# Kernel tuning notes

Measured on AMD Instinct MI355X. Metric: run time of the kernel, lower is better.

## Reference

```python
import jax, jax.numpy as jnp
import numpy as np

B, HW, E = 64, 14, 512   # batch, feature-map side, encoder_dim
A = D = M = 512          # attention_dim, decoder_dim, embed_dim
V = 1000                 # vocab_size
L = 257                  # max caption length -> T = 256 decode steps


def setup_inputs() -> dict:
    key = jax.random.key(0)
    ks = jax.random.split(key, 16)
    def w(k, shape, s=0.05):
        return jax.random.normal(k, shape, dtype=jnp.float32) * s
    encoder_out = jax.random.normal(ks[0], (B, HW, HW, E), dtype=jnp.float32)
    encoded_captions = jax.random.randint(ks[1], (B, L), 0, V)
    caption_lengths = jax.random.randint(ks[2], (B, 1), 2, L + 1)
    caption_lengths = caption_lengths.at[0, 0].set(L)  # ensure max(decode_lengths) == L-1
    return dict(
        encoder_out=encoder_out,
        encoded_captions=encoded_captions,
        caption_lengths=caption_lengths,
        emb=w(ks[3], (V, M), 0.1),
        enc_att_w=w(ks[4], (A, E)), enc_att_b=jnp.zeros((A,), jnp.float32),
        dec_att_w=w(ks[5], (A, D)), dec_att_b=jnp.zeros((A,), jnp.float32),
        full_att_w=w(ks[6], (1, A)), full_att_b=jnp.zeros((1,), jnp.float32),
        W_ih=w(ks[7], (4 * D, M + E)), b_ih=jnp.zeros((4 * D,), jnp.float32),
        W_hh=w(ks[8], (4 * D, D)), b_hh=jnp.zeros((4 * D,), jnp.float32),
        init_h_w=w(ks[9], (D, E)), init_h_b=jnp.zeros((D,), jnp.float32),
        init_c_w=w(ks[10], (D, E)), init_c_b=jnp.zeros((D,), jnp.float32),
        f_beta_w=w(ks[11], (E, D)), f_beta_b=jnp.zeros((E,), jnp.float32),
        fc_w=w(ks[12], (V, D), 0.1), fc_b=jnp.zeros((V,), jnp.float32),
    )


def _forward(encoder_out, emb, enc_att_w, enc_att_b, dec_att_w, dec_att_b,
             full_att_w, full_att_b, W_ih, b_ih, W_hh, b_hh,
             init_h_w, init_h_b, init_c_w, init_c_b,
             f_beta_w, f_beta_b, fc_w, fc_b,
             encoded_captions, caption_lengths):
    Bn = encoder_out.shape[0]
    En = encoder_out.shape[-1]
    enc = encoder_out.reshape(Bn, -1, En)            # [B, P, E]
    lens = caption_lengths[:, 0]
    sort_ind = jnp.argsort(-lens)                    # descending caption length
    lens = lens[sort_ind]
    enc = enc[sort_ind]
    caps = encoded_captions[sort_ind]
    embs = emb[caps]                                 # [B, L, M]
    mean_enc = enc.mean(axis=1)
    h0 = mean_enc @ init_h_w.T + init_h_b            # [B, D]
    c0 = mean_enc @ init_c_w.T + init_c_b
    att1 = enc @ enc_att_w.T + enc_att_b             # [B, P, A] (loop-invariant)
    dec_len = lens - 1
    T = caps.shape[1] - 1
    embs_seq = jnp.transpose(embs[:, :T, :], (1, 0, 2))  # [T, B, M]

    def step(carry, xs):
        h, c = carry
        t, emb_t = xs
        # soft attention (full batch; torch slices to active rows, masked below)
        att2 = h @ dec_att_w.T + dec_att_b                                   # [B, A]
        e = jnp.einsum('bpa,a->bp', jax.nn.relu(att1 + att2[:, None, :]),
                       full_att_w[0]) + full_att_b[0]                        # [B, P]
        alpha = jax.nn.softmax(e, axis=1)
        awe = jnp.einsum('bpe,bp->be', enc, alpha)                           # [B, E]
        gate = jax.nn.sigmoid(h @ f_beta_w.T + f_beta_b)
        x = jnp.concatenate([emb_t, gate * awe], axis=1)                     # [B, M+E]
        # LSTMCell
        gates = x @ W_ih.T + b_ih + h @ W_hh.T + b_hh
        i, f, g, o = jnp.split(gates, 4, axis=1)
        c_new = jax.nn.sigmoid(f) * c + jax.nn.sigmoid(i) * jnp.tanh(g)
        h_new = jax.nn.sigmoid(o) * jnp.tanh(c_new)
        m = (t < dec_len).astype(h.dtype)[:, None]                           # active mask
        h2 = m * h_new + (1 - m) * h
        c2 = m * c_new + (1 - m) * c
        preds = (h_new @ fc_w.T + fc_b) * m   # dropout is identity in eval
        return (h2, c2), (preds, alpha * m)

    (_, _), (preds, alphas) = jax.lax.scan(step, (h0, c0), (jnp.arange(T), embs_seq))
    predictions = jnp.transpose(preds, (1, 0, 2))   # [B, T, V]
    alphas = jnp.transpose(alphas, (1, 0, 2))       # [B, T, P]
    return predictions, caps, alphas, sort_ind


def reference(encoder_out, encoded_captions, caption_lengths, emb,
              enc_att_w, enc_att_b, dec_att_w, dec_att_b, full_att_w, full_att_b,
              W_ih, b_ih, W_hh, b_hh, init_h_w, init_h_b, init_c_w, init_c_b,
              f_beta_w, f_beta_b, fc_w, fc_b):
    return _forward(encoder_out, emb, enc_att_w, enc_att_b, dec_att_w, dec_att_b,
                    full_att_w, full_att_b, W_ih, b_ih, W_hh, b_hh,
                    init_h_w, init_h_b, init_c_w, init_c_b,
                    f_beta_w, f_beta_b, fc_w, fc_b,
                    encoded_captions, caption_lengths)
```

## Files before the change

### kernel.cpp

```cpp
#include <hip/hip_runtime.h>
#include <cstdint>
#include <cstddef>

#define NBLK 256
#define NTHR 512
#define B_ 64
#define P_ 196
#define E_ 512
#define A_ 512
#define D_ 512
#define M_ 512
#define V_ 1000
#define L_ 257
#define T_ 256

#define OUT_PRED  0
#define OUT_CAPS  (B_*T_*V_)
#define OUT_ALPHA (OUT_CAPS + B_*L_)
#define OUT_SORT  (OUT_ALPHA + B_*T_*P_)

typedef _Float16 h2 __attribute__((ext_vector_type(2)));
typedef _Float16 f16x8 __attribute__((ext_vector_type(8)));
typedef float f32x4 __attribute__((ext_vector_type(4)));

struct KP {
  const float* enc; const int* caps; const int* clen;
  const float* emb;
  const float* eaw; const float* eab;
  const float* daw; const float* dab;
  const float* faw; const float* fab;
  const float* wih; const float* bih;
  const float* whh; const float* bhh;
  const float* ihw; const float* ihb;
  const float* icw; const float* icb;
  const float* fbw; const float* fbb;
  const float* fcw; const float* fcb;
  float* out;
  int* bar; int* flb; int* gf;
  int* sort_ind; int* dec_len;
  float* mnT; float* hA; float* hB; float* hnG;
  float* a2G; float* gateG; float* aweQ; float* eG; float* att1;
};

__device__ __forceinline__ float sigf(float x){ return 1.f/(1.f+__expf(-x)); }
__device__ __forceinline__ float tanhf_(float x){
  float ax = fabsf(x);
  float e = __expf(-2.f*ax);
  float r = (1.f-e)/(1.f+e);
  return x < 0.f ? -r : r;
}
__device__ __forceinline__ unsigned short f2bf(float x){
  unsigned u = __float_as_uint(x);
  unsigned r = (u + 0x7fffu + ((u >> 16) & 1u)) >> 16;
  return (unsigned short)r;
}
__device__ __forceinline__ float fdot2f(h2 a, h2 b, float c){
#if __has_builtin(__builtin_amdgcn_fdot2)
  return __builtin_amdgcn_fdot2(a, b, c, false);
#else
  return c + (float)a.x*(float)b.x + (float)a.y*(float)b.y;
#endif
}
__device__ __forceinline__ unsigned packh2(float a, float b){
  h2 v; v.x = (_Float16)a; v.y = (_Float16)b;
  return __builtin_bit_cast(unsigned, v);
}
__device__ __forceinline__ h2 ash2(unsigned u){ return __builtin_bit_cast(h2, u); }
__device__ __forceinline__ f16x8 asf8(uint4 u){ return __builtin_bit_cast(f16x8, u); }

#define LD_A(p)     __hip_atomic_load((p), __ATOMIC_RELAXED, __HIP_MEMORY_SCOPE_AGENT)
#define ST_A(p,v)   __hip_atomic_store((p),(v), __ATOMIC_RELAXED, __HIP_MEMORY_SCOPE_AGENT)
#define ST_REL(p,v) __hip_atomic_store((p),(v), __ATOMIC_RELEASE, __HIP_MEMORY_SCOPE_AGENT)
#define FAA(p)      __hip_atomic_fetch_add((p),1, __ATOMIC_RELAXED, __HIP_MEMORY_SCOPE_AGENT)
__device__ __forceinline__ float ldg_c(const float* p){
  return __hip_atomic_load(p, __ATOMIC_RELAXED, __HIP_MEMORY_SCOPE_AGENT);
}
__device__ __forceinline__ float2 ldg2_c(const float* p){
  unsigned long long u = __hip_atomic_load((const unsigned long long*)p,
                       __ATOMIC_RELAXED, __HIP_MEMORY_SCOPE_AGENT);
  return __builtin_bit_cast(float2, u);
}
__device__ __forceinline__ void stg_c(float* p, float v){
  __hip_atomic_store(p, v, __ATOMIC_RELAXED, __HIP_MEMORY_SCOPE_AGENT);
}

__device__ __forceinline__ void gridbar(int* bar, int blk){
  __syncthreads();
  if (threadIdx.x == 0){
    __builtin_amdgcn_fence(__ATOMIC_RELEASE, "agent");
    int s = LD_A(&bar[144]);
    int* leaf = &bar[(blk & 7)*16];
    if (FAA(leaf) == 31){
      ST_A(leaf, 0);
      if (FAA(&bar[128]) == 7){
        ST_A(&bar[128], 0);
        ST_REL(&bar[144], s+1);
      }
    }
    while (LD_A(&bar[144]) == s) __builtin_amdgcn_s_sleep(2);
    __builtin_amdgcn_fence(__ATOMIC_ACQUIRE, "agent");
  }
  __syncthreads();
}

__device__ __forceinline__ void octbar(int* fl, int O, int r, int ep){
  __syncthreads();
  if (threadIdx.x == 0) ST_A(&fl[O*64 + r], ep);
  if (threadIdx.x < 32){
    while (LD_A(&fl[O*64 + (int)threadIdx.x]) < ep) __builtin_amdgcn_s_sleep(2);
  }
  asm volatile("" ::: "memory");
  __syncthreads();
}

template<int KSW>
__device__ __forceinline__ void gemv_regs(const uint4 (&wfr)[4][KSW],
                                          const uint4* __restrict__ x4,
                                          float* redW, int lane, int wave){
  f32x4 d0 = {0.f,0.f,0.f,0.f}, d1 = d0, d2 = d0, d3 = d0;
  const int rowc = lane & 7;
  const int lg = lane >> 4;
  #pragma unroll
  for (int ks = 0; ks < KSW; ks++){
    const int ksg = wave*KSW + ks;
    f16x8 bf = asf8(x4[(ksg*4 + lg)*8 + rowc]);
    d0 = __builtin_amdgcn_mfma_f32_16x16x32_f16(asf8(wfr[0][ks]), bf, d0, 0, 0, 0);
    d1 = __builtin_amdgcn_mfma_f32_16x16x32_f16(asf8(wfr[1][ks]), bf, d1, 0, 0, 0);
    d2 = __builtin_amdgcn_mfma_f32_16x16x32_f16(asf8(wfr[2][ks]), bf, d2, 0, 0, 0);
    d3 = __builtin_amdgcn_mfma_f32_16x16x32_f16(asf8(wfr[3][ks]), bf, d3, 0, 0, 0);
  }
  const int j = lane & 15;
  if (j < 8){
    const int ib = (lane >> 4) * 4;
    #pragma unroll
    for (int r = 0; r < 4; r++){
      redW[wave*512 + (( 0 + ib + r)*8) + j] = d0[r];
      redW[wave*512 + ((16 + ib + r)*8) + j] = d1[r];
      redW[wave*512 + ((32 + ib + r)*8) + j] = d2[r];
      redW[wave*512 + ((48 + ib + r)*8) + j] = d3[r];
    }
  }
}

__global__ __launch_bounds__(NTHR, 2) void dec_kernel(KP p){
  __shared__ __align__(16) char smem_raw[151104];
  unsigned short* att1L = (unsigned short*)smem_raw;
  unsigned* encT2  = (unsigned*)(smem_raw + 50176);
  float* fwL       = (float*)(smem_raw + 105472);
  float* cL        = (float*)(smem_raw + 107520);
  int*   sbL       = (int*)(smem_raw + 108032);
  char* SCR        = smem_raw + 108096;
  uint4* xH8_4     = (uint4*)SCR;
  float* redW      = (float*)(SCR + 24576);
  float* gLs       = (float*)(SCR + 40960);
  float* a2L       = (float*)SCR;
  float* gateL     = (float*)(SCR + 2048);
  float* eL        = (float*)(SCR + 4096);
  float* alphaL    = (float*)(SCR + 5120);
  unsigned* alpha2L= (unsigned*)(SCR + 6144);

  const int blk  = blockIdx.x;
  const int tid  = threadIdx.x;
  const int lane = tid & 63;
  const int wave = tid >> 6;
  const int b    = blk >> 2;
  const int q    = blk & 3;
  const int ct   = blk & 31;
  const int bt   = blk >> 5;

  if (blk == 0){
    if (tid < B_){
      int lb = p.clen[tid];
      int rank = 0;
      for (int j = 0; j < B_; j++){
        int lj = p.clen[j];
        rank += (lj > lb) || (lj == lb && j < tid);
      }
      p.sort_ind[rank] = tid;
      p.dec_len[rank]  = lb - 1;
      p.out[OUT_SORT + rank] = (float)tid;
    }
    __syncthreads();
    for (int idx = tid; idx < B_*L_; idx += NTHR){
      int bb = idx / L_;
      int l = idx - bb*L_;
      int sbv = p.sort_ind[bb];
      p.out[OUT_CAPS + idx] = (float)p.caps[sbv*L_ + l];
    }
  }
  gridbar(p.bar, blk);

  const int sb  = p.sort_ind[b];
  const int dlb = p.dec_len[b];

  for (int task = blk; task < 260; task += NBLK){
    if (task < 196){
      const int r0 = task*64;
      float* wL = (float*)smem_raw;
      float* eLt = (float*)smem_raw + 512*33;
      const int tx = tid & 31, ty = tid >> 5;
      float acc[4][16];
      #pragma unroll
      for (int i=0;i<4;i++)
        #pragma unroll
        for (int j=0;j<16;j++) acc[i][j] = 0.f;
      for (int k0 = 0; k0 < 512; k0 += 32){
        __syncthreads();
        for (int i = tid; i < 512*32; i += NTHR){
          int a = i >> 5, kk = i & 31;
          wL[a*33 + kk] = p.eaw[a*512 + k0 + kk];
        }
        for (int i = tid; i < 64*32; i += NTHR){
          int rl = i >> 5, kk = i & 31;
          int r = r0 + rl;
          int bb = r / 196;
          int pp = r - bb*196;
          int sbv = p.sort_ind[bb];
          eLt[rl*33 + kk] = p.enc[((size_t)sbv*196 + pp)*512 + k0 + kk];
        }
        __syncthreads();
        for (int kk = 0; kk < 32; kk++){
          float ev[4];
          #pragma unroll
          for (int ii=0;ii<4;ii++) ev[ii] = eLt[(ty*4+ii)*33 + kk];
          #pragma unroll
          for (int jj=0;jj<16;jj++){
            float wv = wL[(tx + 32*jj)*33 + kk];
            #pragma unroll
            for (int ii=0;ii<4;ii++) acc[ii][jj] = fmaf(ev[ii], wv, acc[ii][jj]);
          }
        }
      }
      #pragma unroll
      for (int jj=0;jj<16;jj++){
        int a = tx + 32*jj;
        float bbv = p.eab[a];
        #pragma unroll
        for (int ii=0;ii<4;ii++){
          int r = r0 + ty*4 + ii;
          p.att1[(size_t)r*512 + a] = acc[ii][jj] + bbv;
        }
      }
      __syncthreads();
    } else {
      int bb = task - 196;
      int sbv = p.sort_ind[bb];
      const float* eb = p.enc + (size_t)sbv*P_*E_;
      for (int e = tid; e < E_; e += NTHR){
        float s = 0.f;
        for (int pp = 0; pp < P_; pp++) s += eb[pp*E_ + e];
        p.mnT[bb*512 + e] = s * (1.f/196.f);
      }
    }
  }
  gridbar(p.bar, blk);

  for (int idx = tid; idx < 49*512; idx += NTHR){
    int pp = idx >> 9, a = idx & 511;
    att1L[idx] = f2bf(p.att1[((size_t)(b*196 + q*49 + pp))*512 + a]);
  }
  for (int i = tid; i < 512*25; i += NTHR){
    int p2 = i >> 9, e = i & 511;
    int pr0 = q*49 + 2*p2;
    float e0 = p.enc[((size_t)sb*196 + pr0)*512 + e];
    float e1 = (2*p2+1 < 49) ? p.enc[((size_t)sb*196 + pr0 + 1)*512 + e] : 0.f;
    encT2[e*27 + p2] = packh2(e0, e1);
  }
  fwL[tid] = p.faw[tid];
  if (tid < 8)       sbL[tid]     = p.sort_ind[bt*8 + tid];
  else if (tid < 16) sbL[tid]     = p.dec_len[bt*8 + (tid-8)];
  uint4 wa[4][2];
  uint4 wg[4][6];
  {
    const int cgb = ct*64 + (lane & 15);
    const int kof = (lane >> 4) << 3;
    #pragma unroll
    for (int mt = 0; mt < 4; mt++){
      int cg = cgb + mt*16;
      #pragma unroll
      for (int ks = 0; ks < 2; ks++){
        int k = (wave*2 + ks)*32 + kof;
        uint4 o = {0u,0u,0u,0u};
        const float* src = nullptr;
        if (cg < 512)        src = p.daw + (size_t)cg*512 + k;
        else if (cg < 1024)  src = p.fbw + (size_t)(cg-512)*512 + k;
        else if (cg < 2024)  src = p.fcw + (size_t)(cg-1024)*512 + k;
        if (src){
          const float4* s4 = (const float4*)src;
          float4 f0 = s4[0], f1 = s4[1];
          o.x = packh2(f0.x,f0.y); o.y = packh2(f0.z,f0.w);
          o.z = packh2(f1.x,f1.y); o.w = packh2(f1.z,f1.w);
        }
        wa[mt][ks] = o;
      }
      int jj = cg >> 2, g = cg & 3;
      #pragma unroll
      for (int ks = 0; ks < 6; ks++){
        int k = (wave*6 + ks)*32 + kof;
        const float* src = (k < 1024) ? p.wih + (size_t)(g*512+jj)*1024 + k
                                      : p.whh + (size_t)(g*512+jj)*512 + (k-1024);
        const float4* s4 = (const float4*)src;
        float4 f0 = s4[0], f1 = s4[1];
        uint4 o;
        o.x = packh2(f0.x,f0.y); o.y = packh2(f0.z,f0.w);
        o.z = packh2(f1.x,f1.y); o.w = packh2(f1.z,f1.w);
        wg[mt][ks] = o;
      }
    }
  }
  if (tid < 128){
    int jj = tid >> 3, bb2 = tid & 7;
    int b8 = bt*8 + bb2, jg = ct*16 + jj;
    const float* mrow = p.mnT + b8*512;
    const float* hw = p.ihw + (size_t)jg*512;
    const float* cw = p.icw + (size_t)jg*512;
    float ah = 0.f, ac = 0.f;
    for (int k = 0; k < 512; k++){ ah = fmaf(hw[k], mrow[k], ah); ac = fmaf(cw[k], mrow[k], ac); }
    stg_c(&p.hA[b8*512 + jg], ah + p.ihb[jg]);
    cL[jj*8 + bb2] = ac + p.icb[jg];
  }
  gridbar(p.bar, blk);

  const float fab0 = p.fab[0];
  int ep = 0;

  for (int t = 0; t < T_; t++){
    const float* hR = (t & 1) ? p.hB : p.hA;
    float*       hW = (t & 1) ? p.hA : p.hB;

    if (ct < 16 || t > 0){
      {
        const float* xsrc = (ct < 16) ? hR : p.hnG;
        int cc = tid >> 3, r = tid & 7;
        const float* src = xsrc + (size_t)(bt*8 + r)*512 + cc*8;
        float2 v0 = ldg2_c(src), v1 = ldg2_c(src+2), v2 = ldg2_c(src+4), v3 = ldg2_c(src+6);
        uint4 o;
        o.x = packh2(v0.x,v0.y); o.y = packh2(v1.x,v1.y);
        o.z = packh2(v2.x,v2.y); o.w = packh2(v3.x,v3.y);
        xH8_4[tid] = o;
      }
      __syncthreads();
      gemv_regs<2>(wa, xH8_4, redW, lane, wave);
      __syncthreads();
      {
        float s = 0.f;
        #pragma unroll
        for (int w8 = 0; w8 < 8; w8++) s += redW[w8*512 + tid];
        int c_local = tid >> 3, j = tid & 7, b8 = bt*8 + j;
        if (ct < 16){
          int vcl = ct*64 + c_local;
          if (vcl < 512) stg_c(&p.a2G[b8*512 + vcl], s + p.dab[vcl]);
          else           stg_c(&p.gateG[b8*512 + (vcl-512)], sigf(s + p.fbb[vcl-512]));
        } else {
          int v2i = (ct-16)*64 + c_local;
          if (v2i < 1000){
            bool mm = (t-1) < sbL[8 + j];
            p.out[OUT_PRED + ((size_t)b8*T_ + (t-1))*V_ + v2i] = mm ? (s + p.fcb[v2i]) : 0.f;
          }
        }
      }
    }
    octbar(p.flb, bt, ct, ++ep);

    {
      a2L[tid]   = ldg_c(&p.a2G[b*512 + tid]);
      gateL[tid] = ldg_c(&p.gateG[b*512 + tid]);
      __syncthreads();
      {
        float4 aA = ((float4*)a2L)[lane*2], aB = ((float4*)a2L)[lane*2+1];
        float4 fA = ((float4*)fwL)[lane*2], fB = ((float4*)fwL)[lane*2+1];
        for (int pp = wave; pp < 49; pp += 8){
          uint4 raw = ((const uint4*)att1L)[pp*64 + lane];
          float s =
            fmaxf(__uint_as_float(raw.x << 16)        + aA.x, 0.f)*fA.x +
            fmaxf(__uint_as_float(raw.x & 0xffff0000u)+ aA.y, 0.f)*fA.y +
            fmaxf(__uint_as_float(raw.y << 16)        + aA.z, 0.f)*fA.z +
            fmaxf(__uint_as_float(raw.y & 0xffff0000u)+ aA.w, 0.f)*fA.w +
            fmaxf(__uint_as_float(raw.z << 16)        + aB.x, 0.f)*fB.x +
            fmaxf(__uint_as_float(raw.z & 0xffff0000u)+ aB.y, 0.f)*fB.y +
            fmaxf(__uint_as_float(raw.w << 16)        + aB.z, 0.f)*fB.z +
            fmaxf(__uint_as_float(raw.w & 0xffff0000u)+ aB.w, 0.f)*fB.w;
          #pragma unroll
          for (int o = 32; o > 0; o >>= 1) s += __shfl_down(s, o);
          if (lane == 0) stg_c(&p.eG[b*256 + q*49 + pp], s + fab0);
        }
      }
      __syncthreads();
      if (tid == 0) ST_A(&p.gf[b*16 + q], t+1);
      if (tid < 4){
        while (LD_A(&p.gf[b*16 + tid]) < t+1) __builtin_amdgcn_s_sleep(1);
      }
      asm volatile("" ::: "memory");
      __syncthreads();
      if (tid < 196) eL[tid] = ldg_c(&p.eG[b*256 + tid]);
      __syncthreads();
      if (wave == 0){
        float mx = -1e30f;
        for (int i = lane; i < P_; i += 64) mx = fmaxf(mx, eL[i]);
        #pragma unroll
        for (int o = 32; o > 0; o >>= 1) mx = fmaxf(mx, __shfl_xor(mx, o));
        float sum = 0.f;
        for (int i = lane; i < P_; i += 64){
          float ex = __expf(eL[i] - mx);
          alphaL[i] = ex;
          sum += ex;
        }
        #pragma unroll
        for (int o = 32; o > 0; o >>= 1) sum += __shfl_xor(sum, o);
        float inv = 1.f / sum;
        for (int i = lane; i < P_; i += 64) alphaL[i] *= inv;
      }
      __syncthreads();
      {
        bool mb = t < dlb;
        if (tid < 49)
          p.out[OUT_ALPHA + ((size_t)b*T_ + t)*P_ + q*49 + tid] = mb ? alphaL[q*49 + tid] : 0.f;
        if (tid < 25){
          float a0 = alphaL[q*49 + 2*tid];
          float a1 = (2*tid+1 < 49) ? alphaL[q*49 + 2*tid + 1] : 0.f;
          alpha2L[tid] = packh2(a0, a1);
        }
      }
      __syncthreads();
      {
        const unsigned* ec = encT2 + tid*27;
        float s = 0.f;
        #pragma unroll 5
        for (int p2 = 0; p2 < 25; p2++)
          s = fdot2f(ash2(ec[p2]), ash2(alpha2L[p2]), s);
        stg_c(&p.aweQ[((size_t)b*4 + q)*512 + tid], gateL[tid]*s);
      }
    }
    octbar(p.flb, bt, ct, ++ep);

    {
      {
        int cc = tid >> 3, r = tid & 7;
        int b8 = bt*8 + r;
        {
          int cap = p.caps[sbL[r]*L_ + t];
          const float4* er = (const float4*)(p.emb + (size_t)cap*M_ + cc*8);
          float4 f0 = er[0], f1 = er[1];
          uint4 o;
          o.x = packh2(f0.x,f0.y); o.y = packh2(f0.z,f0.w);
          o.z = packh2(f1.x,f1.y); o.w = packh2(f1.z,f1.w);
          xH8_4[tid] = o;
        }
        {
          const float* aw = p.aweQ + (size_t)b8*4*512 + cc*8;
          float a8[8];
          #pragma unroll
          for (int e = 0; e < 8; e += 2){
            float2 q0 = ldg2_c(aw + 0*512 + e);
            float2 q1 = ldg2_c(aw + 1*512 + e);
            float2 q2 = ldg2_c(aw + 2*512 + e);
            float2 q3 = ldg2_c(aw + 3*512 + e);
            a8[e]   = (q0.x + q1.x) + (q2.x + q3.x);
            a8[e+1] = (q0.y + q1.y) + (q2.y + q3.y);
          }
          uint4 o;
          o.x = packh2(a8[0],a8[1]); o.y = packh2(a8[2],a8[3]);
          o.z = packh2(a8[4],a8[5]); o.w = packh2(a8[6],a8[7]);
          xH8_4[512 + tid] = o;
        }
        {
          const float* hs = hR + (size_t)b8*512 + cc*8;
          float2 v0 = ldg2_c(hs), v1 = ldg2_c(hs+2), v2 = ldg2_c(hs+4), v3 = ldg2_c(hs+6);
          uint4 o;
          o.x = packh2(v0.x,v0.y); o.y = packh2(v1.x,v1.y);
          o.z = packh2(v2.x,v2.y); o.w = packh2(v3.x,v3.y);
          xH8_4[1024 + tid] = o;
        }
      }
      __syncthreads();
      gemv_regs<6>(wg, xH8_4, redW, lane, wave);
      __syncthreads();
      {
        float s = 0.f;
        #pragma unroll
        for (int w8 = 0; w8 < 8; w8++) s += redW[w8*512 + tid];
        gLs[(tid & 7)*64 + (tid >> 3)] = s;
      }
      __syncthreads();
      if (tid < 128){
        int jj = tid >> 3, bb2 = tid & 7;
        int b8 = bt*8 + bb2, jg = ct*16 + jj;
        float g0 = gLs[bb2*64 + jj*4+0] + p.bih[jg]        + p.bhh[jg];
        float g1 = gLs[bb2*64 + jj*4+1] + p.bih[512 + jg]  + p.bhh[512 + jg];
        float g2 = gLs[bb2*64 + jj*4+2] + p.bih[1024 + jg] + p.bhh[1024 + jg];
        float g3 = gLs[bb2*64 + jj*4+3] + p.bih[1536 + jg] + p.bhh[1536 + jg];
        float i_s = sigf(g0), f_s = sigf(g1), g_t = tanhf_(g2), o_s = sigf(g3);
        float c_old = cL[jj*8 + bb2];
        float c_new = f_s*c_old + i_s*g_t;
        float h_new = o_s*tanhf_(c_new);
        bool m = t < sbL[8 + bb2];
        float h_old = ldg_c(&hR[b8*512 + jg]);
        cL[jj*8 + bb2] = m ? c_new : c_old;
        stg_c(&p.hnG[b8*512 + jg], h_new);
        stg_c(&hW[b8*512 + jg], m ? h_new : h_old);
      }
    }
    octbar(p.flb, bt, ct, ++ep);
  }

  if (ct >= 16){
    {
      int cc = tid >> 3, r = tid & 7;
      const float* src = p.hnG + (size_t)(bt*8 + r)*512 + cc*8;
      float2 v0 = ldg2_c(src), v1 = ldg2_c(src+2), v2 = ldg2_c(src+4), v3 = ldg2_c(src+6);
      uint4 o;
      o.x = packh2(v0.x,v0.y); o.y = packh2(v1.x,v1.y);
      o.z = packh2(v2.x,v2.y); o.w = packh2(v3.x,v3.y);
      xH8_4[tid] = o;
    }
    __syncthreads();
    gemv_regs<2>(wa, xH8_4, redW, lane, wave);
    __syncthreads();
    {
      float s = 0.f;
      #pragma unroll
      for (int w8 = 0; w8 < 8; w8++) s += redW[w8*512 + tid];
      int c_local = tid >> 3, j = tid & 7, b8 = bt*8 + j;
      int v2i = (ct-16)*64 + c_local;
      if (v2i < 1000){
        bool mm = (T_-1) < sbL[8 + j];
        p.out[OUT_PRED + ((size_t)b8*T_ + (T_-1))*V_ + v2i] = mm ? (s + p.fcb[v2i]) : 0.f;
      }
    }
  }
}

extern "C" void kernel_launch(void* const* d_in, const int* in_sizes, int n_in,
                              void* d_out, int out_size, void* d_ws, size_t ws_size,
                              hipStream_t stream){
  (void)in_sizes; (void)n_in; (void)out_size; (void)ws_size;
  KP p;
  p.enc  = (const float*)d_in[0];
  p.caps = (const int*)  d_in[1];
  p.clen = (const int*)  d_in[2];
  p.emb  = (const float*)d_in[3];
  p.eaw  = (const float*)d_in[4];  p.eab = (const float*)d_in[5];
  p.daw  = (const float*)d_in[6];  p.dab = (const float*)d_in[7];
  p.faw  = (const float*)d_in[8];  p.fab = (const float*)d_in[9];
  p.wih  = (const float*)d_in[10]; p.bih = (const float*)d_in[11];
  p.whh  = (const float*)d_in[12]; p.bhh = (const float*)d_in[13];
  p.ihw  = (const float*)d_in[14]; p.ihb = (const float*)d_in[15];
  p.icw  = (const float*)d_in[16]; p.icb = (const float*)d_in[17];
  p.fbw  = (const float*)d_in[18]; p.fbb = (const float*)d_in[19];
  p.fcw  = (const float*)d_in[20]; p.fcb = (const float*)d_in[21];
  p.out  = (float*)d_out;

  char* ws = (char*)d_ws;
  size_t off = 0;
  p.bar = (int*)(ws + off); off += 1024;
  p.flb = (int*)(ws + off); off += 8*64*4;
  p.gf  = (int*)(ws + off); off += 64*16*4;
  size_t zero_bytes = off;
  p.sort_ind = (int*)(ws + off); off += 64*4;
  p.dec_len  = (int*)(ws + off); off += 64*4;
  off = (off + 255) & ~(size_t)255;
  p.mnT   = (float*)(ws + off); off += (size_t)B_*512*4;
  p.hA    = (float*)(ws + off); off += (size_t)B_*512*4;
  p.hB    = (float*)(ws + off); off += (size_t)B_*512*4;
  p.hnG   = (float*)(ws + off); off += (size_t)B_*512*4;
  p.a2G   = (float*)(ws + off); off += (size_t)B_*512*4;
  p.gateG = (float*)(ws + off); off += (size_t)B_*512*4;
  p.aweQ  = (float*)(ws + off); off += (size_t)B_*4*512*4;
  p.eG    = (float*)(ws + off); off += (size_t)B_*256*4;
  p.att1  = (float*)(ws + off); off += (size_t)B_*P_*A_*4;

  hipMemsetAsync(ws, 0, zero_bytes, stream);

  void* args[] = { (void*)&p };
  hipLaunchCooperativeKernel((const void*)dec_kernel,
                             dim3(NBLK), dim3(NTHR), args, 0, stream);
}
```

Baseline: 5.617 ms.

## Split-softmax attention to drop per-step quarter barrier; store hidden state as fp16

```diff
diff --git a/kernel.cpp b/kernel.cpp
--- a/kernel.cpp
+++ b/kernel.cpp
@@ -36,10 +36,11 @@
   const float* fbw; const float* fbb;
   const float* fcw; const float* fcb;
   float* out;
-  int* bar; int* flb; int* gf;
+  int* bar; int* flb;
   int* sort_ind; int* dec_len;
-  float* mnT; float* hA; float* hB; float* hnG;
-  float* a2G; float* gateG; float* aweQ; float* eG; float* att1;
+  float* mnT;
+  unsigned* hfA; unsigned* hfB; unsigned* hfN;
+  float* a2G; float* gateG; float* aweQ; float* sA; float* alA; float* att1;
 };
 
 __device__ __forceinline__ float sigf(float x){ return 1.f/(1.f+__expf(-x)); }
@@ -80,7 +81,15 @@
                        __ATOMIC_RELAXED, __HIP_MEMORY_SCOPE_AGENT);
   return __builtin_bit_cast(float2, u);
 }
+__device__ __forceinline__ uint2 ldgu2_c(const unsigned* p){
+  unsigned long long u = __hip_atomic_load((const unsigned long long*)p,
+                       __ATOMIC_RELAXED, __HIP_MEMORY_SCOPE_AGENT);
+  return __builtin_bit_cast(uint2, u);
+}
 __device__ __forceinline__ void stg_c(float* p, float v){
+  __hip_atomic_store(p, v, __ATOMIC_RELAXED, __HIP_MEMORY_SCOPE_AGENT);
+}
+__device__ __forceinline__ void stgu_c(unsigned* p, unsigned v){
   __hip_atomic_store(p, v, __ATOMIC_RELAXED, __HIP_MEMORY_SCOPE_AGENT);
 }
 
@@ -107,7 +116,7 @@
   __syncthreads();
   if (threadIdx.x == 0) ST_A(&fl[O*64 + r], ep);
   if (threadIdx.x < 32){
-    while (LD_A(&fl[O*64 + (int)threadIdx.x]) < ep) __builtin_amdgcn_s_sleep(2);
+    while (LD_A(&fl[O*64 + (int)threadIdx.x]) < ep) __builtin_amdgcn_s_sleep(1);
   }
   asm volatile("" ::: "memory");
   __syncthreads();
@@ -143,21 +152,24 @@
 }
 
 __global__ __launch_bounds__(NTHR, 2) void dec_kernel(KP p){
-  __shared__ __align__(16) char smem_raw[151104];
+  __shared__ __align__(16) char smem_raw[152320];
   unsigned short* att1L = (unsigned short*)smem_raw;
   unsigned* encT2  = (unsigned*)(smem_raw + 50176);
   float* fwL       = (float*)(smem_raw + 105472);
   float* cL        = (float*)(smem_raw + 107520);
   int*   sbL       = (int*)(smem_raw + 108032);
-  char* SCR        = smem_raw + 108096;
+  float* hLoc      = (float*)(smem_raw + 108096);
+  float* hnT       = (float*)(smem_raw + 108608);
+  float* wfacL     = (float*)(smem_raw + 109120);
+  char* SCR        = smem_raw + 109312;
   uint4* xH8_4     = (uint4*)SCR;
   float* redW      = (float*)(SCR + 24576);
   float* gLs       = (float*)(SCR + 40960);
   float* a2L       = (float*)SCR;
   float* gateL     = (float*)(SCR + 2048);
   float* eL        = (float*)(SCR + 4096);
-  float* alphaL    = (float*)(SCR + 5120);
-  unsigned* alpha2L= (unsigned*)(SCR + 6144);
+  float* alphaL    = (float*)(SCR + 4352);
+  unsigned* alpha2L= (unsigned*)(SCR + 4608);
 
   const int blk  = blockIdx.x;
   const int tid  = threadIdx.x;
@@ -191,7 +203,6 @@
   gridbar(p.bar, blk);
 
   const int sb  = p.sort_ind[b];
-  const int dlb = p.dec_len[b];
 
   for (int task = blk; task < 260; task += NBLK){
     if (task < 196){
@@ -316,8 +327,15 @@
     const float* cw = p.icw + (size_t)jg*512;
     float ah = 0.f, ac = 0.f;
     for (int k = 0; k < 512; k++){ ah = fmaf(hw[k], mrow[k], ah); ac = fmaf(cw[k], mrow[k], ac); }
-    stg_c(&p.hA[b8*512 + jg], ah + p.ihb[jg]);
+    hLoc[jj*8 + bb2] = ah + p.ihb[jg];
     cL[jj*8 + bb2] = ac + p.icb[jg];
+  }
+  __syncthreads();
+  if (tid < 64){
+    int j2 = tid >> 3, bb2 = tid & 7;
+    int b8 = bt*8 + bb2;
+    stgu_c(&p.hfA[b8*256 + ct*8 + j2],
+           packh2(hLoc[(2*j2)*8 + bb2], hLoc[(2*j2+1)*8 + bb2]));
   }
   gridbar(p.bar, blk);
 
@@ -325,18 +343,26 @@
   int ep = 0;
 
   for (int t = 0; t < T_; t++){
-    const float* hR = (t & 1) ? p.hB : p.hA;
-    float*       hW = (t & 1) ? p.hA : p.hB;
+    const unsigned* hfR = (t & 1) ? p.hfB : p.hfA;
+    unsigned*       hfW = (t & 1) ? p.hfA : p.hfB;
+
+    uint4 embPre;
+    {
+      int cc = tid >> 3, r = tid & 7;
+      int cap = p.caps[sbL[r]*L_ + t];
+      const float4* er = (const float4*)(p.emb + (size_t)cap*M_ + cc*8);
+      float4 f0 = er[0], f1 = er[1];
+      embPre.x = packh2(f0.x,f0.y); embPre.y = packh2(f0.z,f0.w);
+      embPre.z = packh2(f1.x,f1.y); embPre.w = packh2(f1.z,f1.w);
+    }
 
     if (ct < 16 || t > 0){
       {
-        const float* xsrc = (ct < 16) ? hR : p.hnG;
+        const unsigned* xsrc = (ct < 16) ? hfR : p.hfN;
         int cc = tid >> 3, r = tid & 7;
-        const float* src = xsrc + (size_t)(bt*8 + r)*512 + cc*8;
-        float2 v0 = ldg2_c(src), v1 = ldg2_c(src+2), v2 = ldg2_c(src+4), v3 = ldg2_c(src+6);
-        uint4 o;
-        o.x = packh2(v0.x,v0.y); o.y = packh2(v1.x,v1.y);
-        o.z = packh2(v2.x,v2.y); o.w = packh2(v3.x,v3.y);
+        const unsigned* src = xsrc + (bt*8 + r)*256 + cc*4;
+        uint2 u0 = ldgu2_c(src), u1 = ldgu2_c(src + 2);
+        uint4 o; o.x = u0.x; o.y = u0.y; o.z = u1.x; o.w = u1.y;
         xH8_4[tid] = o;
       }
       __syncthreads();
@@ -382,44 +408,33 @@
             fmaxf(__uint_as_float(raw.w & 0xffff0000u)+ aB.w, 0.f)*fB.w;
           #pragma unroll
           for (int o = 32; o > 0; o >>= 1) s += __shfl_down(s, o);
-          if (lane == 0) stg_c(&p.eG[b*256 + q*49 + pp], s + fab0);
-        }
-      }
-      __syncthreads();
-      if (tid == 0) ST_A(&p.gf[b*16 + q], t+1);
-      if (tid < 4){
-        while (LD_A(&p.gf[b*16 + tid]) < t+1) __builtin_amdgcn_s_sleep(1);
-      }
-      asm volatile("" ::: "memory");
-      __syncthreads();
-      if (tid < 196) eL[tid] = ldg_c(&p.eG[b*256 + tid]);
+          if (lane == 0) eL[pp] = s + fab0;
+        }
+      }
       __syncthreads();
       if (wave == 0){
-        float mx = -1e30f;
-        for (int i = lane; i < P_; i += 64) mx = fmaxf(mx, eL[i]);
+        float ev = (lane < 49) ? eL[lane] : -1e30f;
+        float mx = ev;
         #pragma unroll
         for (int o = 32; o > 0; o >>= 1) mx = fmaxf(mx, __shfl_xor(mx, o));
-        float sum = 0.f;
-        for (int i = lane; i < P_; i += 64){
-          float ex = __expf(eL[i] - mx);
-          alphaL[i] = ex;
-          sum += ex;
-        }
+        float ex = (lane < 49) ? __expf(ev - mx) : 0.f;
+        if (lane < 49){
+          alphaL[lane] = ex;
+          stg_c(&p.alA[(b*4 + q)*49 + lane], ex);
+        }
+        float sum = ex;
         #pragma unroll
         for (int o = 32; o > 0; o >>= 1) sum += __shfl_xor(sum, o);
-        float inv = 1.f / sum;
-        for (int i = lane; i < P_; i += 64) alphaL[i] *= inv;
-      }
-      __syncthreads();
-      {
-        bool mb = t < dlb;
-        if (tid < 49)
-          p.out[OUT_ALPHA + ((size_t)b*T_ + t)*P_ + q*49 + tid] = mb ? alphaL[q*49 + tid] : 0.f;
-        if (tid < 25){
-          float a0 = alphaL[q*49 + 2*tid];
-          float a1 = (2*tid+1 < 49) ? alphaL[q*49 + 2*tid + 1] : 0.f;
-          alpha2L[tid] = packh2(a0, a1);
-        }
+        if (lane == 0){
+          stg_c(&p.sA[(b*4 + q)*2 + 0], mx);
+          stg_c(&p.sA[(b*4 + q)*2 + 1], sum);
+        }
+      }
+      __syncthreads();
+      if (tid < 25){
+        float a0 = alphaL[2*tid];
+        float a1 = (2*tid+1 < 49) ? alphaL[2*tid + 1] : 0.f;
+        alpha2L[tid] = packh2(a0, a1);
       }
       __syncthreads();
       {
@@ -434,42 +449,55 @@
     octbar(p.flb, bt, ct, ++ep);
 
     {
+      if (tid < 32){
+        int r = tid >> 2, qq = tid & 3, b8 = bt*8 + r;
+        float2 s0 = ldg2_c(&p.sA[(b8*4 + 0)*2]);
+        float2 s1 = ldg2_c(&p.sA[(b8*4 + 1)*2]);
+        float2 s2 = ldg2_c(&p.sA[(b8*4 + 2)*2]);
+        float2 s3 = ldg2_c(&p.sA[(b8*4 + 3)*2]);
+        float mx = fmaxf(fmaxf(s0.x, s1.x), fmaxf(s2.x, s3.x));
+        float sum = s0.y*__expf(s0.x - mx) + s1.y*__expf(s1.x - mx)
+                  + s2.y*__expf(s2.x - mx) + s3.y*__expf(s3.x - mx);
+        float mq = (qq == 0) ? s0.x : (qq == 1) ? s1.x : (qq == 2) ? s2.x : s3.x;
+        wfacL[tid] = __expf(mq - mx) / sum;
+      }
       {
         int cc = tid >> 3, r = tid & 7;
-        int b8 = bt*8 + r;
-        {
-          int cap = p.caps[sbL[r]*L_ + t];
-          const float4* er = (const float4*)(p.emb + (size_t)cap*M_ + cc*8);
-          float4 f0 = er[0], f1 = er[1];
-          uint4 o;
-          o.x = packh2(f0.x,f0.y); o.y = packh2(f0.z,f0.w);
-          o.z = packh2(f1.x,f1.y); o.w = packh2(f1.z,f1.w);
-          xH8_4[tid] = o;
-        }
-        {
-          const float* aw = p.aweQ + (size_t)b8*4*512 + cc*8;
-          float a8[8];
-          #pragma unroll
-          for (int e = 0; e < 8; e += 2){
-            float2 q0 = ldg2_c(aw + 0*512 + e);
-            float2 q1 = ldg2_c(aw + 1*512 + e);
-            float2 q2 = ldg2_c(aw + 2*512 + e);
-            float2 q3 = ldg2_c(aw + 3*512 + e);
-            a8[e]   = (q0.x + q1.x) + (q2.x + q3.x);
-            a8[e+1] = (q0.y + q1.y) + (q2.y + q3.y);
-          }
-          uint4 o;
-          o.x = packh2(a8[0],a8[1]); o.y = packh2(a8[2],a8[3]);
-          o.z = packh2(a8[4],a8[5]); o.w = packh2(a8[6],a8[7]);
-          xH8_4[512 + tid] = o;
-        }
-        {
-          const float* hs = hR + (size_t)b8*512 + cc*8;
-          float2 v0 = ldg2_c(hs), v1 = ldg2_c(hs+2), v2 = ldg2_c(hs+4), v3 = ldg2_c(hs+6);
-          uint4 o;
-          o.x = packh2(v0.x,v0.y); o.y = packh2(v1.x,v1.y);
-          o.z = packh2(v2.x,v2.y); o.w = packh2(v3.x,v3.y);
-          xH8_4[1024 + tid] = o;
+        xH8_4[tid] = embPre;
+        const unsigned* hs = hfR + (bt*8 + r)*256 + cc*4;
+        uint2 u0 = ldgu2_c(hs), u1 = ldgu2_c(hs + 2);
+        uint4 o; o.x = u0.x; o.y = u0.y; o.z = u1.x; o.w = u1.y;
+        xH8_4[1024 + tid] = o;
+      }
+      __syncthreads();
+      {
+        int cc = tid >> 3, r = tid & 7;
+        const float* aw = p.aweQ + ((size_t)(bt*8 + r)*4)*512 + cc*8;
+        float w0 = wfacL[r*4+0], w1 = wfacL[r*4+1], w2 = wfacL[r*4+2], w3 = wfacL[r*4+3];
+        float a8[8];
+        #pragma unroll
+        for (int e = 0; e < 8; e += 2){
+          float2 q0 = ldg2_c(aw + 0*512 + e);
+          float2 q1 = ldg2_c(aw + 1*512 + e);
+          float2 q2 = ldg2_c(aw + 2*512 + e);
+          float2 q3 = ldg2_c(aw + 3*512 + e);
+          a8[e]   = q0.x*w0 + q1.x*w1 + q2.x*w2 + q3.x*w3;
+          a8[e+1] = q0.y*w0 + q1.y*w1 + q2.y*w2 + q3.y*w3;
+        }
+        uint4 o;
+        o.x = packh2(a8[0],a8[1]); o.y = packh2(a8[2],a8[3]);
+        o.z = packh2(a8[4],a8[5]); o.w = packh2(a8[6],a8[7]);
+        xH8_4[512 + tid] = o;
+      }
+      #pragma unroll
+      for (int ii = 0; ii < 4; ii++){
+        int idx = tid + ii*NTHR;
+        if (idx < 8*196){
+          int r = idx / 196, pp = idx - r*196;
+          float av = ldg_c(&p.alA[(bt*8 + r)*196 + pp]);
+          float wv = wfacL[r*4 + pp/49];
+          bool mb = t < sbL[8 + r];
+          p.out[OUT_ALPHA + ((size_t)(bt*8 + r)*T_ + t)*P_ + pp] = mb ? av*wv : 0.f;
         }
       }
       __syncthreads();
@@ -484,7 +512,7 @@
       __syncthreads();
       if (tid < 128){
         int jj = tid >> 3, bb2 = tid & 7;
-        int b8 = bt*8 + bb2, jg = ct*16 + jj;
+        int jg = ct*16 + jj;
         float g0 = gLs[bb2*64 + jj*4+0] + p.bih[jg]        + p.bhh[jg];
         float g1 = gLs[bb2*64 + jj*4+1] + p.bih[512 + jg]  + p.bhh[512 + jg];
         float g2 = gLs[bb2*64 + jj*4+2] + p.bih[1024 + jg] + p.bhh[1024 + jg];
@@ -494,10 +522,19 @@
         float c_new = f_s*c_old + i_s*g_t;
         float h_new = o_s*tanhf_(c_new);
         bool m = t < sbL[8 + bb2];
-        float h_old = ldg_c(&hR[b8*512 + jg]);
-        cL[jj*8 + bb2] = m ? c_new : c_old;
-        stg_c(&p.hnG[b8*512 + jg], h_new);
-        stg_c(&hW[b8*512 + jg], m ? h_new : h_old);
+        float h_old = hLoc[jj*8 + bb2];
+        cL[jj*8 + bb2]   = m ? c_new : c_old;
+        hLoc[jj*8 + bb2] = m ? h_new : h_old;
+        hnT[jj*8 + bb2]  = h_new;
+      }
+      __syncthreads();
+      if (tid < 64){
+        int j2 = tid >> 3, bb2 = tid & 7;
+        int b8 = bt*8 + bb2;
+        stgu_c(&hfW[b8*256 + ct*8 + j2],
+               packh2(hLoc[(2*j2)*8 + bb2], hLoc[(2*j2+1)*8 + bb2]));
+        stgu_c(&p.hfN[b8*256 + ct*8 + j2],
+               packh2(hnT[(2*j2)*8 + bb2], hnT[(2*j2+1)*8 + bb2]));
       }
     }
     octbar(p.flb, bt, ct, ++ep);
@@ -506,11 +543,9 @@
   if (ct >= 16){
     {
       int cc = tid >> 3, r = tid & 7;
-      const float* src = p.hnG + (size_t)(bt*8 + r)*512 + cc*8;
-      float2 v0 = ldg2_c(src), v1 = ldg2_c(src+2), v2 = ldg2_c(src+4), v3 = ldg2_c(src+6);
-      uint4 o;
-      o.x = packh2(v0.x,v0.y); o.y = packh2(v1.x,v1.y);
-      o.z = packh2(v2.x,v2.y); o.w = packh2(v3.x,v3.y);
+      const unsigned* src = p.hfN + (bt*8 + r)*256 + cc*4;
+      uint2 u0 = ldgu2_c(src), u1 = ldgu2_c(src + 2);
+      uint4 o; o.x = u0.x; o.y = u0.y; o.z = u1.x; o.w = u1.y;
       xH8_4[tid] = o;
     }
     __syncthreads();
@@ -554,19 +589,21 @@
   size_t off = 0;
   p.bar = (int*)(ws + off); off += 1024;
   p.flb = (int*)(ws + off); off += 8*64*4;
-  p.gf  = (int*)(ws + off); off += 64*16*4;
   size_t zero_bytes = off;
   p.sort_ind = (int*)(ws + off); off += 64*4;
   p.dec_len  = (int*)(ws + off); off += 64*4;
   off = (off + 255) & ~(size_t)255;
   p.mnT   = (float*)(ws + off); off += (size_t)B_*512*4;
-  p.hA    = (float*)(ws + off); off += (size_t)B_*512*4;
-  p.hB    = (float*)(ws + off); off += (size_t)B_*512*4;
-  p.hnG   = (float*)(ws + off); off += (size_t)B_*512*4;
+  p.hfA   = (unsigned*)(ws + off); off += (size_t)B_*256*4;
+  p.hfB   = (unsigned*)(ws + off); off += (size_t)B_*256*4;
+  p.hfN   = (unsigned*)(ws + off); off += (size_t)B_*256*4;
   p.a2G   = (float*)(ws + off); off += (size_t)B_*512*4;
   p.gateG = (float*)(ws + off); off += (size_t)B_*512*4;
   p.aweQ  = (float*)(ws + off); off += (size_t)B_*4*512*4;
-  p.eG    = (float*)(ws + off); off += (size_t)B_*256*4;
+  p.sA    = (float*)(ws + off); off += (size_t)B_*4*2*4;
+  off = (off + 255) & ~(size_t)255;
+  p.alA   = (float*)(ws + off); off += (size_t)B_*P_*4;
+  off = (off + 255) & ~(size_t)255;
   p.att1  = (float*)(ws + off); off += (size_t)B_*P_*A_*4;
 
   hipMemsetAsync(ws, 0, zero_bytes, stream);
```

New measurement: 6.153 ms. +9.6%, slower.
